# Kernel tuning notes

Measured on AMD Instinct MI355X. Metric: run time of the kernel, lower is better.

Reference implementation:

```python
import jax, jax.numpy as jnp
import numpy as np


def _branch(x2d, V, U, v2, v1, u2, u1):
    # x2d: [N, in]; V: [s, in]; U: [out, s]; scales are [1, dim]
    Vq = jnp.sign(V)
    Uq = jnp.sign(U)
    v1u2 = v1 * u2  # [1, s]
    h = (x2d * v2) @ Vq.T          # [N, s]
    y = (h * v1u2) @ Uq.T          # [N, out]
    return y * u1


def setup_inputs() -> dict:
    key = jax.random.key(0)
    ks = jax.random.split(key, 14)
    IN, OUT, S = 4096, 4096, 1024
    B, T = 4, 2048
    f = jax.random.normal
    return {
        "x":    f(ks[0], (B, T, IN), jnp.float32),
        "V":    f(ks[1], (S, IN), jnp.float32),
        "U":    f(ks[2], (OUT, S), jnp.float32),
        "v2":   f(ks[3], (1, IN), jnp.float32),
        "v1":   f(ks[4], (1, S), jnp.float32),
        "u2":   f(ks[5], (1, S), jnp.float32),
        "u1":   f(ks[6], (1, OUT), jnp.float32),
        "V_R":  f(ks[7], (S, IN), jnp.float32),
        "U_R":  f(ks[8], (OUT, S), jnp.float32),
        "v2_R": f(ks[9], (1, IN), jnp.float32),
        "v1_R": f(ks[10], (1, S), jnp.float32),
        "u2_R": f(ks[11], (1, S), jnp.float32),
        "u1_R": f(ks[12], (1, OUT), jnp.float32),
        "bias": f(ks[13], (OUT,), jnp.float32),
    }


def reference(x, V, U, v2, v1, u2, u1, V_R, U_R, v2_R, v1_R, u2_R, u1_R, bias):
    *lead, hidden = x.shape
    x2d = x.reshape(-1, hidden)
    y = _branch(x2d, V, U, v2, v1, u2, u1)
    y = y + _branch(x2d, V_R, U_R, v2_R, v1_R, u2_R, u1_R)
    y = y + bias
    return y.reshape(*lead, bias.shape[0])
```

## Files before the change

kernel.cpp:

```cpp
#include <hip/hip_runtime.h>
#include <hip/hip_bf16.h>
#include <stdint.h>

typedef __bf16 bf16_t;
typedef __attribute__((ext_vector_type(8))) __bf16 bf16x8;
typedef __attribute__((ext_vector_type(4))) float f32x4;

#define DIM_IN  4096
#define DIM_OUT 4096
#define DIM_S   1024
#define DIM_S2  2048
#define NROWS   8192

typedef const __attribute__((address_space(1))) void gvoid_t;
typedef __attribute__((address_space(3))) void lvoid_t;

__device__ __forceinline__ float signf(float v) {
    return (v > 0.f) ? 1.f : ((v < 0.f) ? -1.f : 0.f);
}


__global__ void cast_x_kernel(const float* __restrict__ x, bf16_t* __restrict__ xb) {
    int idx = blockIdx.x * blockDim.x + threadIdx.x;
    const float4* p = reinterpret_cast<const float4*>(x) + (size_t)idx * 2;
    float4 a = p[0], b = p[1];
    bf16x8 o;
    o[0] = (bf16_t)a.x; o[1] = (bf16_t)a.y; o[2] = (bf16_t)a.z; o[3] = (bf16_t)a.w;
    o[4] = (bf16_t)b.x; o[5] = (bf16_t)b.y; o[6] = (bf16_t)b.z; o[7] = (bf16_t)b.w;
    reinterpret_cast<bf16x8*>(xb)[idx] = o;
}

__global__ void build_vcat_kernel(const float* __restrict__ V, const float* __restrict__ v2,
                                  const float* __restrict__ V_R, const float* __restrict__ v2_R,
                                  bf16_t* __restrict__ out) {
    int idx = blockIdx.x * blockDim.x + threadIdx.x;
    int s2 = idx >> 9;
    int i0 = (idx & 511) * 8;
    const float* src; const float* sc;
    if (s2 < DIM_S) { src = V   + (size_t)s2 * DIM_IN;           sc = v2;   }
    else            { src = V_R + (size_t)(s2 - DIM_S) * DIM_IN; sc = v2_R; }
    float4 a  = *reinterpret_cast<const float4*>(src + i0);
    float4 b  = *reinterpret_cast<const float4*>(src + i0 + 4);
    float4 sa = *reinterpret_cast<const float4*>(sc + i0);
    float4 sb = *reinterpret_cast<const float4*>(sc + i0 + 4);
    bf16x8 o;
    o[0] = (bf16_t)(signf(a.x) * sa.x); o[1] = (bf16_t)(signf(a.y) * sa.y);
    o[2] = (bf16_t)(signf(a.z) * sa.z); o[3] = (bf16_t)(signf(a.w) * sa.w);
    o[4] = (bf16_t)(signf(b.x) * sb.x); o[5] = (bf16_t)(signf(b.y) * sb.y);
    o[6] = (bf16_t)(signf(b.z) * sb.z); o[7] = (bf16_t)(signf(b.w) * sb.w);
    reinterpret_cast<bf16x8*>(out)[idx] = o;
}

__global__ void build_wcat_kernel(const float* __restrict__ U, const float* __restrict__ v1,
                                  const float* __restrict__ u2, const float* __restrict__ u1,
                                  const float* __restrict__ U_R, const float* __restrict__ v1_R,
                                  const float* __restrict__ u2_R, const float* __restrict__ u1_R,
                                  bf16_t* __restrict__ out) {
    int idx = blockIdx.x * blockDim.x + threadIdx.x;
    int j  = idx >> 8;
    int s0 = (idx & 255) * 8;
    const float* srcU; const float* sv1; const float* su2; float amp;
    if (s0 < DIM_S) { srcU = U   + (size_t)j * DIM_S + s0; sv1 = v1 + s0;   su2 = u2 + s0;   amp = u1[j];   }
    else { int s = s0 - DIM_S;
           srcU = U_R + (size_t)j * DIM_S + s;  sv1 = v1_R + s; su2 = u2_R + s; amp = u1_R[j]; }
    float4 a  = *reinterpret_cast<const float4*>(srcU);
    float4 b  = *reinterpret_cast<const float4*>(srcU + 4);
    float4 va = *reinterpret_cast<const float4*>(sv1);
    float4 vb = *reinterpret_cast<const float4*>(sv1 + 4);
    float4 ua = *reinterpret_cast<const float4*>(su2);
    float4 ub = *reinterpret_cast<const float4*>(su2 + 4);
    bf16x8 o;
    o[0] = (bf16_t)(amp * va.x * ua.x * signf(a.x));
    o[1] = (bf16_t)(amp * va.y * ua.y * signf(a.y));
    o[2] = (bf16_t)(amp * va.z * ua.z * signf(a.z));
    o[3] = (bf16_t)(amp * va.w * ua.w * signf(a.w));
    o[4] = (bf16_t)(amp * vb.x * ub.x * signf(b.x));
    o[5] = (bf16_t)(amp * vb.y * ub.y * signf(b.y));
    o[6] = (bf16_t)(amp * vb.z * ub.z * signf(b.z));
    o[7] = (bf16_t)(amp * vb.w * ub.w * signf(b.w));
    reinterpret_cast<bf16x8*>(out)[idx] = o;
}


#define VMCNT(n) do { asm volatile("s_waitcnt vmcnt(" #n ")" ::: "memory"); \
                      __builtin_amdgcn_sched_barrier(0); } while (0)

template<int N, int K, bool OUT_BF16>
__global__ __launch_bounds__(512, 2) void gemm256_kernel(
        const bf16_t* __restrict__ A, const bf16_t* __restrict__ B,
        bf16_t* __restrict__ Cb, float* __restrict__ Cf,
        const float* __restrict__ bias) {
    extern __shared__ char lds[];
    constexpr int NT = K / 64;
    const int tid  = threadIdx.x;
    const int wave = tid >> 6;
    const int lane = tid & 63;
    const int wr = wave >> 2;
    const int wc = wave & 3;

    const int nwg  = gridDim.x;
    const int orig = blockIdx.x;
    const int swz  = (orig & 7) * (nwg >> 3) + (orig >> 3);
    constexpr int NTX = N / 256;
    const int n0 = (swz % NTX) * 256;
    const int m0 = (swz / NTX) * 256;

    char* ldsA = lds;
    char* ldsB = lds + 65536;

    const char* gA[2]; const char* gB[2];
#pragma unroll
    for (int j = 0; j < 2; ++j) {
        int off = j * 8192 + wave * 1024 + lane * 16;
        int lg  = off ^ (((off >> 7) & 3) << 4);
        int row = lg >> 6;
        int cb  = lg & 63;
        gA[j] = (const char*)A + (size_t)(m0 + row) * (K * 2) + cb;
        gB[j] = (const char*)B + (size_t)(n0 + row) * (K * 2) + cb;
    }

#define STAGE_A(t, kh) do { \
    int _lo = (((t) & 1) << 15) + ((kh) << 14) + (wave << 10); \
    int _ga = (t) * 128 + (kh) * 64; \
    __builtin_amdgcn_global_load_lds((gvoid_t*)(gA[0] + _ga), (lvoid_t*)(ldsA + _lo), 16, 0, 0); \
    __builtin_amdgcn_global_load_lds((gvoid_t*)(gA[1] + _ga), (lvoid_t*)(ldsA + _lo + 8192), 16, 0, 0); \
} while (0)
#define STAGE_B(t, kh) do { \
    int _lo = (((t) & 1) << 15) + ((kh) << 14) + (wave << 10); \
    int _ga = (t) * 128 + (kh) * 64; \
    __builtin_amdgcn_global_load_lds((gvoid_t*)(gB[0] + _ga), (lvoid_t*)(ldsB + _lo), 16, 0, 0); \
    __builtin_amdgcn_global_load_lds((gvoid_t*)(gB[1] + _ga), (lvoid_t*)(ldsB + _lo + 8192), 16, 0, 0); \
} while (0)

    STAGE_A(0, 0); STAGE_B(0, 0);
    STAGE_A(0, 1); STAGE_B(0, 1);
    STAGE_A(1, 0); STAGE_B(1, 0);

    int aoff[8], boff[4];
#pragma unroll
    for (int m = 0; m < 8; ++m) {
        int row = wr * 128 + m * 16 + (lane & 15);
        int off = row * 64 + ((lane >> 4) << 4);
        aoff[m] = off ^ (((off >> 7) & 3) << 4);
    }
#pragma unroll
    for (int n = 0; n < 4; ++n) {
        int row = wc * 64 + n * 16 + (lane & 15);
        int off = row * 64 + ((lane >> 4) << 4);
        boff[n] = off ^ (((off >> 7) & 3) << 4);
    }

    f32x4 acc[8][4];
#pragma unroll
    for (int m = 0; m < 8; ++m)
#pragma unroll
        for (int n = 0; n < 4; ++n)
            acc[m][n] = (f32x4){0.f, 0.f, 0.f, 0.f};

    bf16x8 bfr[4];

    VMCNT(8);
    __builtin_amdgcn_s_barrier();

#define PHASE(mh, kh, LOADB, STG, VMS) do { \
    const int _sb = ((t & 1) << 15) + ((kh) << 14); \
    bf16x8 _af[4]; \
    _Pragma("unroll") \
    for (int mi = 0; mi < 4; ++mi) \
        _af[mi] = *(const bf16x8*)(ldsA + _sb + aoff[(mh) * 4 + mi]); \
    if (LOADB) { \
        _Pragma("unroll") \
        for (int n = 0; n < 4; ++n) \
            bfr[n] = *(const bf16x8*)(ldsB + _sb + boff[n]); \
    } \
    STG; \
    __builtin_amdgcn_s_barrier(); \
    asm volatile("s_waitcnt lgkmcnt(0)" ::: "memory"); \
    __builtin_amdgcn_sched_barrier(0); \
    __builtin_amdgcn_s_setprio(1); \
    _Pragma("unroll") \
    for (int mi = 0; mi < 4; ++mi) \
        _Pragma("unroll") \
        for (int n = 0; n < 4; ++n) \
            acc[(mh) * 4 + mi][n] = __builtin_amdgcn_mfma_f32_16x16x32_bf16( \
                _af[mi], bfr[n], acc[(mh) * 4 + mi][n], 0, 0, 0); \
    __builtin_amdgcn_s_setprio(0); \
    VMS; \
    __builtin_amdgcn_s_barrier(); \
} while (0)

    for (int t = 0; t < NT; ++t) {
        const bool i1 = (t + 1 < NT);
        const bool i2 = (t + 2 < NT);
        PHASE(0, 0, true,  { if (i1) STAGE_A(t + 1, 1); }, {});
        PHASE(1, 0, false, { if (i1) STAGE_B(t + 1, 1); },
              { if (i1) VMCNT(8); else VMCNT(0); });
        PHASE(0, 1, true,  { if (i2) STAGE_A(t + 2, 0); }, {});
        PHASE(1, 1, false, { if (i2) STAGE_B(t + 2, 0); },
              { if (i2) VMCNT(8); else VMCNT(4); });
    }

#undef PHASE
#undef STAGE_A
#undef STAGE_B

    const int cr = (lane >> 4) << 2;
    const int cc = lane & 15;
#pragma unroll
    for (int m = 0; m < 8; ++m) {
        const int row = m0 + wr * 128 + m * 16 + cr;
#pragma unroll
        for (int n = 0; n < 4; ++n) {
            const int col = n0 + wc * 64 + n * 16 + cc;
            if (OUT_BF16) {
#pragma unroll
                for (int j = 0; j < 4; ++j)
                    Cb[(size_t)(row + j) * N + col] = (bf16_t)acc[m][n][j];
            } else {
                const float bv = bias[col];
#pragma unroll
                for (int j = 0; j < 4; ++j)
                    Cf[(size_t)(row + j) * N + col] = acc[m][n][j] + bv;
            }
        }
    }
}

extern "C" void kernel_launch(void* const* d_in, const int* in_sizes, int n_in,
                              void* d_out, int out_size, void* d_ws, size_t ws_size,
                              hipStream_t stream) {
    const float* x    = (const float*)d_in[0];
    const float* V    = (const float*)d_in[1];
    const float* U    = (const float*)d_in[2];
    const float* v2   = (const float*)d_in[3];
    const float* v1   = (const float*)d_in[4];
    const float* u2   = (const float*)d_in[5];
    const float* u1   = (const float*)d_in[6];
    const float* V_R  = (const float*)d_in[7];
    const float* U_R  = (const float*)d_in[8];
    const float* v2_R = (const float*)d_in[9];
    const float* v1_R = (const float*)d_in[10];
    const float* u2_R = (const float*)d_in[11];
    const float* u1_R = (const float*)d_in[12];
    const float* bias = (const float*)d_in[13];
    float* out = (float*)d_out;

    char* ws = (char*)d_ws;
    bf16_t* Xb   = (bf16_t*)(ws);
    bf16_t* Vcat = (bf16_t*)(ws + (size_t)64  * 1024 * 1024);
    bf16_t* Wcat = (bf16_t*)(ws + (size_t)80  * 1024 * 1024);
    bf16_t* Hb   = (bf16_t*)(ws + (size_t)96  * 1024 * 1024);

    (void)hipFuncSetAttribute((const void*)gemm256_kernel<DIM_S2, DIM_IN, true>,
                              hipFuncAttributeMaxDynamicSharedMemorySize, 131072);
    (void)hipFuncSetAttribute((const void*)gemm256_kernel<DIM_OUT, DIM_S2, false>,
                              hipFuncAttributeMaxDynamicSharedMemorySize, 131072);

    cast_x_kernel    <<<16384, 256, 0, stream>>>(x, Xb);
    build_vcat_kernel<<<4096, 256, 0, stream>>>(V, v2, V_R, v2_R, Vcat);
    build_wcat_kernel<<<4096, 256, 0, stream>>>(U, v1, u2, u1, U_R, v1_R, u2_R, u1_R, Wcat);

    gemm256_kernel<DIM_S2, DIM_IN, true>
        <<<(DIM_S2 / 256) * (NROWS / 256), 512, 131072, stream>>>(Xb, Vcat, Hb, nullptr, nullptr);
    gemm256_kernel<DIM_OUT, DIM_S2, false>
        <<<(DIM_OUT / 256) * (NROWS / 256), 512, 131072, stream>>>(Hb, Wcat, nullptr, out, bias);
}
```

Baseline: 312.4 us.

## Double-buffer LDS fragment reads to overlap with MFMA in GEMM main loop

Restructures the GEMM k-loop so the LDS reads for the next phase's A/B fragments go into alternate register buffers while the current phase's MFMAs run. Partial lgkmcnt waits replace the full drain. The loop is peeled for the last two tiles, and per-fragment offset arrays become a single base plus constant strides. This is meant to hide LDS read latency behind matrix-core work, at the cost of more VGPRs and more delicate wait-count bookkeeping.

```diff
diff --git a/kernel.cpp b/kernel.cpp
--- a/kernel.cpp
+++ b/kernel.cpp
@@ -84,6 +84,8 @@
 
 #define VMCNT(n) do { asm volatile("s_waitcnt vmcnt(" #n ")" ::: "memory"); \
                       __builtin_amdgcn_sched_barrier(0); } while (0)
+#define LGKM(n)  do { asm volatile("s_waitcnt lgkmcnt(" #n ")" ::: "memory"); \
+                      __builtin_amdgcn_sched_barrier(0); } while (0)
 
 template<int N, int K, bool OUT_BF16>
 __global__ __launch_bounds__(512, 2) void gemm256_kernel(
@@ -92,6 +94,7 @@
         const float* __restrict__ bias) {
     extern __shared__ char lds[];
     constexpr int NT = K / 64;
+    static_assert(NT >= 4, "K too small");
     const int tid  = threadIdx.x;
     const int wave = tid >> 6;
     const int lane = tid & 63;
@@ -132,22 +135,12 @@
     __builtin_amdgcn_global_load_lds((gvoid_t*)(gB[1] + _ga), (lvoid_t*)(ldsB + _lo + 8192), 16, 0, 0); \
 } while (0)
 
-    STAGE_A(0, 0); STAGE_B(0, 0);
-    STAGE_A(0, 1); STAGE_B(0, 1);
-    STAGE_A(1, 0); STAGE_B(1, 0);
-
-    int aoff[8], boff[4];
-#pragma unroll
-    for (int m = 0; m < 8; ++m) {
-        int row = wr * 128 + m * 16 + (lane & 15);
-        int off = row * 64 + ((lane >> 4) << 4);
-        aoff[m] = off ^ (((off >> 7) & 3) << 4);
-    }
-#pragma unroll
-    for (int n = 0; n < 4; ++n) {
-        int row = wc * 64 + n * 16 + (lane & 15);
-        int off = row * 64 + ((lane >> 4) << 4);
-        boff[n] = off ^ (((off >> 7) & 3) << 4);
+    int abase, bbase;
+    {
+        int offA = (wr * 128 + (lane & 15)) * 64 + ((lane >> 4) << 4);
+        abase = offA ^ (((offA >> 7) & 3) << 4);
+        int offB = (wc * 64 + (lane & 15)) * 64 + ((lane >> 4) << 4);
+        bbase = offB ^ (((offB >> 7) & 3) << 4);
     }
 
     f32x4 acc[8][4];
@@ -157,50 +150,79 @@
         for (int n = 0; n < 4; ++n)
             acc[m][n] = (f32x4){0.f, 0.f, 0.f, 0.f};
 
-    bf16x8 bfr[4];
-
-    VMCNT(8);
-    __builtin_amdgcn_s_barrier();
-
-#define PHASE(mh, kh, LOADB, STG, VMS) do { \
-    const int _sb = ((t & 1) << 15) + ((kh) << 14); \
-    bf16x8 _af[4]; \
+    bf16x8 af0[4], af1[4], bf0[4], bf1[4];
+
+#define RD_A4(dst, mh, kh, t_) do { \
+    const int _sb = (((t_) & 1) << 15) + ((kh) << 14) + abase + (mh) * 4096; \
     _Pragma("unroll") \
     for (int mi = 0; mi < 4; ++mi) \
-        _af[mi] = *(const bf16x8*)(ldsA + _sb + aoff[(mh) * 4 + mi]); \
-    if (LOADB) { \
-        _Pragma("unroll") \
-        for (int n = 0; n < 4; ++n) \
-            bfr[n] = *(const bf16x8*)(ldsB + _sb + boff[n]); \
-    } \
-    STG; \
-    __builtin_amdgcn_s_barrier(); \
-    asm volatile("s_waitcnt lgkmcnt(0)" ::: "memory"); \
-    __builtin_amdgcn_sched_barrier(0); \
+        dst[mi] = *(const bf16x8*)(ldsA + _sb + mi * 1024); \
+} while (0)
+#define RD_B4(dst, kh, t_) do { \
+    const int _sb = (((t_) & 1) << 15) + ((kh) << 14) + bbase; \
+    _Pragma("unroll") \
+    for (int ni = 0; ni < 4; ++ni) \
+        dst[ni] = *(const bf16x8*)(ldsB + _sb + ni * 1024); \
+} while (0)
+#define MFMA16(mh, AF, BF) do { \
     __builtin_amdgcn_s_setprio(1); \
     _Pragma("unroll") \
     for (int mi = 0; mi < 4; ++mi) \
         _Pragma("unroll") \
         for (int n = 0; n < 4; ++n) \
             acc[(mh) * 4 + mi][n] = __builtin_amdgcn_mfma_f32_16x16x32_bf16( \
-                _af[mi], bfr[n], acc[(mh) * 4 + mi][n], 0, 0, 0); \
+                AF[mi], BF[n], acc[(mh) * 4 + mi][n], 0, 0, 0); \
     __builtin_amdgcn_s_setprio(0); \
-    VMS; \
-    __builtin_amdgcn_s_barrier(); \
-} while (0)
-
-    for (int t = 0; t < NT; ++t) {
-        const bool i1 = (t + 1 < NT);
-        const bool i2 = (t + 2 < NT);
-        PHASE(0, 0, true,  { if (i1) STAGE_A(t + 1, 1); }, {});
-        PHASE(1, 0, false, { if (i1) STAGE_B(t + 1, 1); },
-              { if (i1) VMCNT(8); else VMCNT(0); });
-        PHASE(0, 1, true,  { if (i2) STAGE_A(t + 2, 0); }, {});
-        PHASE(1, 1, false, { if (i2) STAGE_B(t + 2, 0); },
-              { if (i2) VMCNT(8); else VMCNT(4); });
-    }
-
-#undef PHASE
+} while (0)
+
+    STAGE_A(0, 0); STAGE_B(0, 0);
+    STAGE_A(0, 1); STAGE_B(0, 1);
+    STAGE_A(1, 0); STAGE_B(1, 0);
+    VMCNT(8);
+    __builtin_amdgcn_s_barrier();
+    RD_A4(af0, 0, 0, 0); RD_B4(bf0, 0, 0);
+
+#define KTILE(t_, I1, I2) do { \
+     \
+    RD_A4(af1, 1, 0, t_); \
+    if (I1) STAGE_A((t_) + 1, 1); \
+    __builtin_amdgcn_s_barrier(); \
+    LGKM(4); \
+    MFMA16(0, af0, bf0); \
+    if (I1) { VMCNT(6); } else { VMCNT(0); } \
+    __builtin_amdgcn_s_barrier(); \
+     \
+    RD_A4(af0, 0, 1, t_); RD_B4(bf1, 1, t_); \
+    if (I1) STAGE_B((t_) + 1, 1); \
+    __builtin_amdgcn_s_barrier(); \
+    LGKM(8); \
+    MFMA16(1, af1, bf0); \
+    __builtin_amdgcn_s_barrier(); \
+     \
+    RD_A4(af1, 1, 1, t_); \
+    if (I2) STAGE_A((t_) + 2, 0); \
+    __builtin_amdgcn_s_barrier(); \
+    LGKM(4); \
+    MFMA16(0, af0, bf1); \
+    if (I2) { VMCNT(6); } else if (I1) { VMCNT(4); } else { VMCNT(0); } \
+    __builtin_amdgcn_s_barrier(); \
+     \
+    if (I1) { RD_A4(af0, 0, 0, (t_) + 1); RD_B4(bf0, 0, (t_) + 1); } \
+    if (I2) STAGE_B((t_) + 2, 0); \
+    __builtin_amdgcn_s_barrier(); \
+    if (I1) { LGKM(8); } else { LGKM(0); } \
+    MFMA16(1, af1, bf1); \
+    __builtin_amdgcn_s_barrier(); \
+} while (0)
+
+    for (int t = 0; t < NT - 2; ++t) KTILE(t, true, true);
+    KTILE(NT - 2, true, false);
+    KTILE(NT - 1, false, false);
+
+#undef KTILE
+#undef RD_A4
+#undef RD_B4
+#undef MFMA16
 #undef STAGE_A
 #undef STAGE_B
 
```

Result: no change. 309.2 us (-1.0%).

## Restructure GEMM LDS layout to 128-byte rows with a single-barrier pipeline

Applied to the files above, without the earlier changes.

Changes the LDS tile layout from two 64-column k-halves to 128-byte rows with an 8-way XOR swizzle, splitting the tile by M/N halves instead. The main loop now uses one barrier per k-tile instead of eight, and waits on vmcnt(0) at the end of each iteration. Global-to-LDS staging for tile t+1 is issued while the MFMAs for tile t run. The aim is to cut barrier and wait overhead, at the cost of a shallower prefetch depth (one tile ahead instead of fractional stages) that may expose memory latency.

```diff
diff --git a/kernel.cpp b/kernel.cpp
--- a/kernel.cpp
+++ b/kernel.cpp
@@ -82,7 +82,7 @@
 }
 
 
-#define VMCNT(n) do { asm volatile("s_waitcnt vmcnt(" #n ")" ::: "memory"); \
+#define VMCNT0() do { asm volatile("s_waitcnt vmcnt(0)" ::: "memory"); \
                       __builtin_amdgcn_sched_barrier(0); } while (0)
 
 template<int N, int K, bool OUT_BF16>
@@ -92,6 +92,7 @@
         const float* __restrict__ bias) {
     extern __shared__ char lds[];
     constexpr int NT = K / 64;
+    static_assert(NT >= 2, "K too small");
     const int tid  = threadIdx.x;
     const int wave = tid >> 6;
     const int lane = tid & 63;
@@ -112,95 +113,95 @@
 #pragma unroll
     for (int j = 0; j < 2; ++j) {
         int off = j * 8192 + wave * 1024 + lane * 16;
-        int lg  = off ^ (((off >> 7) & 3) << 4);
-        int row = lg >> 6;
-        int cb  = lg & 63;
+        int lg  = off ^ (((off >> 7) & 7) << 4);
+        int row = lg >> 7;
+        int cb  = lg & 127;
         gA[j] = (const char*)A + (size_t)(m0 + row) * (K * 2) + cb;
         gB[j] = (const char*)B + (size_t)(n0 + row) * (K * 2) + cb;
     }
 
-#define STAGE_A(t, kh) do { \
-    int _lo = (((t) & 1) << 15) + ((kh) << 14) + (wave << 10); \
-    int _ga = (t) * 128 + (kh) * 64; \
+#define STAGE_A(t_, mh) do { \
+    int _lo = (((t_) & 1) << 15) + ((mh) << 14) + (wave << 10); \
+    size_t _ga = (size_t)(mh) * (128 * K * 2) + (size_t)(t_) * 128; \
     __builtin_amdgcn_global_load_lds((gvoid_t*)(gA[0] + _ga), (lvoid_t*)(ldsA + _lo), 16, 0, 0); \
     __builtin_amdgcn_global_load_lds((gvoid_t*)(gA[1] + _ga), (lvoid_t*)(ldsA + _lo + 8192), 16, 0, 0); \
 } while (0)
-#define STAGE_B(t, kh) do { \
-    int _lo = (((t) & 1) << 15) + ((kh) << 14) + (wave << 10); \
-    int _ga = (t) * 128 + (kh) * 64; \
+#define STAGE_B(t_, nh) do { \
+    int _lo = (((t_) & 1) << 15) + ((nh) << 14) + (wave << 10); \
+    size_t _ga = (size_t)(nh) * (128 * K * 2) + (size_t)(t_) * 128; \
     __builtin_amdgcn_global_load_lds((gvoid_t*)(gB[0] + _ga), (lvoid_t*)(ldsB + _lo), 16, 0, 0); \
     __builtin_amdgcn_global_load_lds((gvoid_t*)(gB[1] + _ga), (lvoid_t*)(ldsB + _lo + 8192), 16, 0, 0); \
 } while (0)
 
-    STAGE_A(0, 0); STAGE_B(0, 0);
-    STAGE_A(0, 1); STAGE_B(0, 1);
-    STAGE_A(1, 0); STAGE_B(1, 0);
-
-    int aoff[8], boff[4];
-#pragma unroll
-    for (int m = 0; m < 8; ++m) {
-        int row = wr * 128 + m * 16 + (lane & 15);
-        int off = row * 64 + ((lane >> 4) << 4);
-        aoff[m] = off ^ (((off >> 7) & 3) << 4);
-    }
-#pragma unroll
-    for (int n = 0; n < 4; ++n) {
-        int row = wc * 64 + n * 16 + (lane & 15);
-        int off = row * 64 + ((lane >> 4) << 4);
-        boff[n] = off ^ (((off >> 7) & 3) << 4);
-    }
-
-    f32x4 acc[8][4];
-#pragma unroll
-    for (int m = 0; m < 8; ++m)
-#pragma unroll
-        for (int n = 0; n < 4; ++n)
-            acc[m][n] = (f32x4){0.f, 0.f, 0.f, 0.f};
-
-    bf16x8 bfr[4];
-
-    VMCNT(8);
-    __builtin_amdgcn_s_barrier();
-
-#define PHASE(mh, kh, LOADB, STG, VMS) do { \
-    const int _sb = ((t & 1) << 15) + ((kh) << 14); \
-    bf16x8 _af[4]; \
+    const int swzmask = (lane & 7) << 4;
+    int abase0, abase1, bbase0, bbase1;
+    {
+        int araw = (lane & 15) * 128 + ((lane >> 4) << 4);
+        abase0 = (araw ^ swzmask) + (wr << 14);
+        abase1 = ((araw + 64) ^ swzmask) + (wr << 14);
+        int braw = ((wc & 1) * 64 + (lane & 15)) * 128 + ((lane >> 4) << 4);
+        bbase0 = (braw ^ swzmask) + ((wc >> 1) << 14);
+        bbase1 = ((braw + 64) ^ swzmask) + ((wc >> 1) << 14);
+    }
+
+#define RD_A4(dst, base, mg, t_) do { \
+    const int _sb = (((t_) & 1) << 15) + (base); \
     _Pragma("unroll") \
     for (int mi = 0; mi < 4; ++mi) \
-        _af[mi] = *(const bf16x8*)(ldsA + _sb + aoff[(mh) * 4 + mi]); \
-    if (LOADB) { \
-        _Pragma("unroll") \
-        for (int n = 0; n < 4; ++n) \
-            bfr[n] = *(const bf16x8*)(ldsB + _sb + boff[n]); \
-    } \
-    STG; \
-    __builtin_amdgcn_s_barrier(); \
-    asm volatile("s_waitcnt lgkmcnt(0)" ::: "memory"); \
-    __builtin_amdgcn_sched_barrier(0); \
+        dst[mi] = *(const bf16x8*)(ldsA + _sb + ((mg) * 4 + mi) * 2048); \
+} while (0)
+#define RD_B4(dst, base, t_) do { \
+    const int _sb = (((t_) & 1) << 15) + (base); \
+    _Pragma("unroll") \
+    for (int ni = 0; ni < 4; ++ni) \
+        dst[ni] = *(const bf16x8*)(ldsB + _sb + ni * 2048); \
+} while (0)
+#define MFMA16(mg, AF, BF) do { \
     __builtin_amdgcn_s_setprio(1); \
     _Pragma("unroll") \
     for (int mi = 0; mi < 4; ++mi) \
         _Pragma("unroll") \
         for (int n = 0; n < 4; ++n) \
-            acc[(mh) * 4 + mi][n] = __builtin_amdgcn_mfma_f32_16x16x32_bf16( \
-                _af[mi], bfr[n], acc[(mh) * 4 + mi][n], 0, 0, 0); \
+            acc[(mg) * 4 + mi][n] = __builtin_amdgcn_mfma_f32_16x16x32_bf16( \
+                AF[mi], BF[n], acc[(mg) * 4 + mi][n], 0, 0, 0); \
     __builtin_amdgcn_s_setprio(0); \
-    VMS; \
-    __builtin_amdgcn_s_barrier(); \
-} while (0)
+} while (0)
+
+    f32x4 acc[8][4];
+#pragma unroll
+    for (int m = 0; m < 8; ++m)
+#pragma unroll
+        for (int n = 0; n < 4; ++n)
+            acc[m][n] = (f32x4){0.f, 0.f, 0.f, 0.f};
+
+    bf16x8 afA[4], afB[4], bf0[4], bf1[4];
+
+    STAGE_A(0, 0); STAGE_A(0, 1);
+    STAGE_B(0, 0); STAGE_B(0, 1);
+    VMCNT0();
+    __builtin_amdgcn_s_barrier();
 
     for (int t = 0; t < NT; ++t) {
         const bool i1 = (t + 1 < NT);
-        const bool i2 = (t + 2 < NT);
-        PHASE(0, 0, true,  { if (i1) STAGE_A(t + 1, 1); }, {});
-        PHASE(1, 0, false, { if (i1) STAGE_B(t + 1, 1); },
-              { if (i1) VMCNT(8); else VMCNT(0); });
-        PHASE(0, 1, true,  { if (i2) STAGE_A(t + 2, 0); }, {});
-        PHASE(1, 1, false, { if (i2) STAGE_B(t + 2, 0); },
-              { if (i2) VMCNT(8); else VMCNT(4); });
-    }
-
-#undef PHASE
+        RD_A4(afA, abase0, 0, t);
+        RD_B4(bf0, bbase0, t);
+        if (i1) { STAGE_A(t + 1, 0); STAGE_A(t + 1, 1); }
+        MFMA16(0, afA, bf0);
+        RD_A4(afB, abase0, 1, t);
+        if (i1) { STAGE_B(t + 1, 0); STAGE_B(t + 1, 1); }
+        MFMA16(1, afB, bf0);
+        RD_A4(afA, abase1, 0, t);
+        RD_B4(bf1, bbase1, t);
+        MFMA16(0, afA, bf1);
+        RD_A4(afB, abase1, 1, t);
+        MFMA16(1, afB, bf1);
+        if (i1) { VMCNT0(); }
+        __builtin_amdgcn_s_barrier();
+    }
+
+#undef RD_A4
+#undef RD_B4
+#undef MFMA16
 #undef STAGE_A
 #undef STAGE_B
 
```

Result: faster. 289.8 us (-7.2%).
